# Kernel optimization log

Hardware: AMD Instinct MI355X
Metric: run time of the kernel (lower is better)

## Reference

```python
import jax, jax.numpy as jnp
import numpy as np

N_NODES = 100000
N_EDGES = 3200000
DROP_P = 0.5


def gcn_conv(x, W, b, src, dst, deg_inv_sqrt, n):
    # PyG GCNConv with self-loops already folded into (src, dst):
    # out[j] = sum_{(i->j)} dinv[i]*dinv[j] * (x W)[i] + b
    h = x @ W
    norm = deg_inv_sqrt[src] * deg_inv_sqrt[dst]          # [E+N]
    msg = h[src] * norm[:, None]                          # [E+N, d_out]
    out = jax.ops.segment_sum(msg, dst, num_segments=n)
    return out + b


def dropout(x, key, p=DROP_P):
    keep = jax.random.bernoulli(key, 1.0 - p, x.shape)
    return jnp.where(keep, x / (1.0 - p), 0.0)


def setup_inputs() -> dict:
    key = jax.random.key(0)
    ks = jax.random.split(key, 8)
    x = jax.random.normal(ks[0], (N_NODES, 64), dtype=jnp.float32)
    edge_index = jax.random.randint(ks[1], (2, N_EDGES), 0, N_NODES, dtype=jnp.int64)
    def glorot(k, fin, fout):
        lim = float(np.sqrt(6.0 / (fin + fout)))
        return jax.random.uniform(k, (fin, fout), jnp.float32, -lim, lim)
    return {
        "x": x,
        "edge_index": edge_index,
        "W1": glorot(ks[2], 64, 32), "b1": jnp.zeros((32,), jnp.float32),
        "W2": glorot(ks[3], 32, 64), "b2": jnp.zeros((64,), jnp.float32),
        "W3": glorot(ks[4], 64, 32), "b3": jnp.zeros((32,), jnp.float32),
    }


def reference(x, edge_index, W1, b1, W2, b2, W3, b3):
    n = x.shape[0]
    loops = jnp.arange(n, dtype=edge_index.dtype)
    src = jnp.concatenate([edge_index[0], loops])          # [E+N]
    dst = jnp.concatenate([edge_index[1], loops])
    deg = jax.ops.segment_sum(jnp.ones_like(dst, dtype=x.dtype), dst, num_segments=n)
    deg_inv_sqrt = jnp.where(deg > 0, jax.lax.rsqrt(deg), 0.0)

    dkey = jax.random.key(42)
    k1, k2 = jax.random.split(dkey)

    h = gcn_conv(x, W1, b1, src, dst, deg_inv_sqrt, n)
    h = jax.nn.celu(h)
    h = dropout(h, k1)
    h = gcn_conv(h, W2, b2, src, dst, deg_inv_sqrt, n)
    h = jax.nn.celu(h)
    h = dropout(h, k2)
    h = gcn_conv(h, W3, b3, src, dst, deg_inv_sqrt, n)
    return jax.nn.celu(h)
```

## Files before the change

kernel.cpp:

```cpp
#include <hip/hip_runtime.h>
#include <stdint.h>
#include <stddef.h>

typedef _Float16 half_t;
typedef _Float16 half4 __attribute__((ext_vector_type(4)));

__host__ __device__ __forceinline__ uint32_t rotl32(uint32_t v, uint32_t r) {
  return (v << r) | (v >> (32u - r));
}

__host__ __device__ __forceinline__ void tf2x32(uint32_t k0, uint32_t k1,
                                                uint32_t x0, uint32_t x1,
                                                uint32_t& o0, uint32_t& o1) {
  uint32_t ks2 = k0 ^ k1 ^ 0x1BD11BDAu;
  x0 += k0; x1 += k1;
  x0 += x1; x1 = rotl32(x1, 13); x1 ^= x0;
  x0 += x1; x1 = rotl32(x1, 15); x1 ^= x0;
  x0 += x1; x1 = rotl32(x1, 26); x1 ^= x0;
  x0 += x1; x1 = rotl32(x1, 6);  x1 ^= x0;
  x0 += k1; x1 += ks2 + 1u;
  x0 += x1; x1 = rotl32(x1, 17); x1 ^= x0;
  x0 += x1; x1 = rotl32(x1, 29); x1 ^= x0;
  x0 += x1; x1 = rotl32(x1, 16); x1 ^= x0;
  x0 += x1; x1 = rotl32(x1, 24); x1 ^= x0;
  x0 += ks2; x1 += k0 + 2u;
  x0 += x1; x1 = rotl32(x1, 13); x1 ^= x0;
  x0 += x1; x1 = rotl32(x1, 15); x1 ^= x0;
  x0 += x1; x1 = rotl32(x1, 26); x1 ^= x0;
  x0 += x1; x1 = rotl32(x1, 6);  x1 ^= x0;
  x0 += k0; x1 += k1 + 3u;
  x0 += x1; x1 = rotl32(x1, 17); x1 ^= x0;
  x0 += x1; x1 = rotl32(x1, 29); x1 ^= x0;
  x0 += x1; x1 = rotl32(x1, 16); x1 ^= x0;
  x0 += x1; x1 = rotl32(x1, 24); x1 ^= x0;
  x0 += k1; x1 += ks2 + 4u;
  x0 += x1; x1 = rotl32(x1, 13); x1 ^= x0;
  x0 += x1; x1 = rotl32(x1, 15); x1 ^= x0;
  x0 += x1; x1 = rotl32(x1, 26); x1 ^= x0;
  x0 += x1; x1 = rotl32(x1, 6);  x1 ^= x0;
  x0 += ks2; x1 += k0 + 5u;
  o0 = x0; o1 = x1;
}

__device__ __forceinline__ bool tf_keep(uint32_t k0, uint32_t k1, uint32_t idx) {
  uint32_t o0, o1;
  tf2x32(k0, k1, 0u, idx, o0, o1);
  return ((o0 ^ o1) >> 31) == 0u;
}

#define CHUNK 4096
#define STASH 5120

__global__ __launch_bounds__(1024) void zero1024(uint32_t* __restrict__ p) {
  p[threadIdx.x] = 0u;
}

__global__ __launch_bounds__(256) void k4_binhist(const int* __restrict__ src,
                                                  const int* __restrict__ dst,
                                                  uint32_t* __restrict__ tbl,
                                                  uint32_t* __restrict__ gbcnt,
                                                  uint32_t* __restrict__ staging,
                                                  int E, int NB) {
  __shared__ uint32_t lcur[1024];
  __shared__ uint32_t ls[256];
  __shared__ uint32_t stage[CHUNK];
  int tid = threadIdx.x;
  for (int i = tid; i < NB; i += 256) lcur[i] = 0u;
  __syncthreads();
  int base = blockIdx.x * CHUNK;
  int end = min(base + CHUNK, E);
  uint32_t dv[16], sv[16];
  int m = 0;
  for (int i = base + tid; i < end; i += 256) {
    dv[m] = (uint32_t)dst[i];
    sv[m] = (uint32_t)src[i];
    ++m;
  }
  for (int q = 0; q < m; ++q) atomicAdd(&lcur[dv[q] >> 7], 1u);
  __syncthreads();
  uint32_t carry = 0u;
  for (int seg = 0; seg < 1024; seg += 256) {
    int i = seg + tid;
    uint32_t v = (i < NB) ? lcur[i] : 0u;
    ls[tid] = v;
    __syncthreads();
    for (int off = 1; off < 256; off <<= 1) {
      uint32_t t = (tid >= off) ? ls[tid - off] : 0u;
      __syncthreads();
      if (tid >= off) ls[tid] += t;
      __syncthreads();
    }
    uint32_t excl = carry + ls[tid] - v;
    if (i < NB) {
      tbl[(size_t)blockIdx.x * NB + i] = (excl << 16) | v;
      if (v) atomicAdd(&gbcnt[i], v);
      lcur[i] = excl;
    }
    carry += ls[255];
    __syncthreads();
  }
  for (int q = 0; q < m; ++q) {
    uint32_t d = dv[q];
    uint32_t p = atomicAdd(&lcur[d >> 7], 1u);
    stage[p] = ((d & 127u) << 17) | sv[q];
  }
  __syncthreads();
  int cnt_total = end - base;
  uint32_t* outp = staging + (size_t)blockIdx.x * CHUNK;
  for (int i = tid; i < cnt_total; i += 256) outp[i] = stage[i];
}

__global__ __launch_bounds__(1024) void k3_bscan(const uint32_t* __restrict__ gbcnt,
                                                 uint32_t* __restrict__ bbase, int NB) {
  __shared__ uint32_t s[1024];
  int i = threadIdx.x;
  uint32_t v = (i < NB) ? gbcnt[i] : 0u;
  s[i] = v;
  __syncthreads();
  for (int off = 1; off < 1024; off <<= 1) {
    uint32_t t = (i >= off) ? s[i - off] : 0u;
    __syncthreads();
    if (i >= off) s[i] += t;
    __syncthreads();
  }
  if (i < NB) bbase[i] = s[i] - v;
}

__global__ __launch_bounds__(256) void k5_fin(
    const uint32_t* __restrict__ staging, const uint32_t* __restrict__ tbl,
    const uint32_t* __restrict__ bbase, uint32_t* __restrict__ rowp,
    float* __restrict__ dinv, uint32_t* __restrict__ esrc,
    int n, int E, int NBLK, int NB) {
  __shared__ uint32_t lpak[1024];
  __shared__ uint32_t P[1025];
  __shared__ uint32_t ls[256];
  __shared__ uint32_t stash[STASH];
  __shared__ uint32_t lc[128];
  __shared__ uint32_t sc[128];
  __shared__ uint32_t lcur[128];
  int tid = threadIdx.x;
  int b = blockIdx.x;
  if (tid < 128) lc[tid] = 0u;
  uint32_t carry = 0u;
  for (int seg = 0; seg < 1024; seg += 256) {
    int i = seg + tid;
    uint32_t packed = (i < NBLK) ? tbl[(size_t)i * NB + b] : 0u;
    lpak[i] = packed;
    uint32_t v = packed & 0xFFFFu;
    ls[tid] = v;
    __syncthreads();
    for (int off = 1; off < 256; off <<= 1) {
      uint32_t t = (tid >= off) ? ls[tid - off] : 0u;
      __syncthreads();
      if (tid >= off) ls[tid] += t;
      __syncthreads();
    }
    P[i] = carry + ls[tid] - v;
    carry += ls[255];
    __syncthreads();
  }
  if (tid == 0) P[NBLK] = carry;
  __syncthreads();
  uint32_t total = P[NBLK];
  for (int i = tid; i < NBLK; i += 256) {
    uint32_t packed = lpak[i];
    uint32_t cnt = packed & 0xFFFFu;
    uint32_t loff = packed >> 16;
    uint32_t p = P[i];
    const uint32_t* run = staging + (size_t)i * CHUNK + loff;
    for (uint32_t t2 = 0; t2 < cnt; ++t2) {
      uint32_t e = run[t2];
      uint32_t q = p + t2;
      if (q < STASH) stash[q] = e;
      atomicAdd(&lc[e >> 17], 1u);
    }
  }
  __syncthreads();
  uint32_t myc = (tid < 128) ? lc[tid] : 0u;
  if (tid < 128) sc[tid] = myc;
  __syncthreads();
  for (int off = 1; off < 128; off <<= 1) {
    uint32_t t = (tid < 128 && tid >= off) ? sc[tid - off] : 0u;
    __syncthreads();
    if (tid < 128 && tid >= off) sc[tid] += t;
    __syncthreads();
  }
  uint32_t s = bbase[b];
  if (tid < 128) {
    uint32_t gstart = s + sc[tid] - myc;
    int node = (b << 7) + tid;
    if (node < n) {
      rowp[node] = gstart;
      dinv[node] = 1.0f / sqrtf((float)(myc + 1u));
    }
    lcur[tid] = gstart;
  }
  if (b == 0 && tid == 0) rowp[n] = (uint32_t)E;
  __syncthreads();
  uint32_t lim = total < (uint32_t)STASH ? total : (uint32_t)STASH;
  for (uint32_t q = tid; q < lim; q += 256) {
    uint32_t e = stash[q];
    uint32_t pos = atomicAdd(&lcur[e >> 17], 1u);
    esrc[pos] = e & 0x1FFFFu;
  }
  if (total > (uint32_t)STASH) {
    for (int i = tid; i < NBLK; i += 256) {
      uint32_t packed = lpak[i];
      uint32_t cnt = packed & 0xFFFFu;
      uint32_t loff = packed >> 16;
      uint32_t p = P[i];
      const uint32_t* run = staging + (size_t)i * CHUNK + loff;
      for (uint32_t t2 = 0; t2 < cnt; ++t2) {
        uint32_t q = p + t2;
        if (q >= (uint32_t)STASH) {
          uint32_t e = run[t2];
          uint32_t pos = atomicAdd(&lcur[e >> 17], 1u);
          esrc[pos] = e & 0x1FFFFu;
        }
      }
    }
  }
}

__global__ __launch_bounds__(256) void gemm_n64_k32(
    const float* __restrict__ X, const float* __restrict__ W,
    const float* __restrict__ dinv, half_t* __restrict__ out16, int n) {
  __shared__ float Ws[64 * 32];
  __shared__ float Xs[32 * 68];
  int tid = threadIdx.x;
  {
    const float4* Wv = (const float4*)W;
    float4* Wsv = (float4*)Ws;
    Wsv[tid] = Wv[tid];
    Wsv[tid + 256] = Wv[tid + 256];
  }
  int row0 = blockIdx.x * 32;
  {
    const float4* Xv = (const float4*)(X + (size_t)row0 * 64);
    int lim = (n - row0) * 16;
    float4 z = make_float4(0.f, 0.f, 0.f, 0.f);
    int i0 = tid, i1 = tid + 256;
    float4 v0 = (i0 < lim) ? Xv[i0] : z;
    float4 v1 = (i1 < lim) ? Xv[i1] : z;
    *(float4*)(Xs + (i0 >> 4) * 68 + ((i0 & 15) << 2)) = v0;
    *(float4*)(Xs + (i1 >> 4) * 68 + ((i1 & 15) << 2)) = v1;
  }
  __syncthreads();
  int r = tid >> 3;
  int c4 = (tid & 7) << 2;
  int row = row0 + r;
  if (row >= n) return;
  float4 acc = make_float4(0.f, 0.f, 0.f, 0.f);
#pragma unroll
  for (int k = 0; k < 64; k += 4) {
    float4 xv = *(const float4*)(Xs + r * 68 + k);
    float4 w0 = *(const float4*)(Ws + (k + 0) * 32 + c4);
    float4 w1 = *(const float4*)(Ws + (k + 1) * 32 + c4);
    float4 w2 = *(const float4*)(Ws + (k + 2) * 32 + c4);
    float4 w3 = *(const float4*)(Ws + (k + 3) * 32 + c4);
    acc.x = fmaf(xv.x, w0.x, acc.x); acc.y = fmaf(xv.x, w0.y, acc.y);
    acc.z = fmaf(xv.x, w0.z, acc.z); acc.w = fmaf(xv.x, w0.w, acc.w);
    acc.x = fmaf(xv.y, w1.x, acc.x); acc.y = fmaf(xv.y, w1.y, acc.y);
    acc.z = fmaf(xv.y, w1.z, acc.z); acc.w = fmaf(xv.y, w1.w, acc.w);
    acc.x = fmaf(xv.z, w2.x, acc.x); acc.y = fmaf(xv.z, w2.y, acc.y);
    acc.z = fmaf(xv.z, w2.z, acc.z); acc.w = fmaf(xv.z, w2.w, acc.w);
    acc.x = fmaf(xv.w, w3.x, acc.x); acc.y = fmaf(xv.w, w3.y, acc.y);
    acc.z = fmaf(xv.w, w3.z, acc.z); acc.w = fmaf(xv.w, w3.w, acc.w);
  }
  float dj = dinv[row];
  half4 h;
  h.x = (half_t)(acc.x * dj); h.y = (half_t)(acc.y * dj);
  h.z = (half_t)(acc.z * dj); h.w = (half_t)(acc.w * dj);
  *(half4*)(out16 + (size_t)row * 32 + c4) = h;
}

__global__ __launch_bounds__(256) void gemm_k32_n64_act(
    const float* __restrict__ X, const float* __restrict__ W,
    const float* __restrict__ bias, float* __restrict__ out,
    uint32_t k0, uint32_t k1, int n) {
  __shared__ float Ws[32 * 64];
  __shared__ float Xs[16 * 36];
  int tid = threadIdx.x;
  {
    const float4* Wv = (const float4*)W;
    float4* Wsv = (float4*)Ws;
    Wsv[tid] = Wv[tid];
    Wsv[tid + 256] = Wv[tid + 256];
  }
  int row0 = blockIdx.x * 16;
  if (tid < 128) {
    const float4* Xv = (const float4*)(X + (size_t)row0 * 32);
    int lim = (n - row0) * 8;
    float4 z = make_float4(0.f, 0.f, 0.f, 0.f);
    float4 v = (tid < lim) ? Xv[tid] : z;
    *(float4*)(Xs + (tid >> 3) * 36 + ((tid & 7) << 2)) = v;
  }
  __syncthreads();
  int r = tid >> 4;
  int c4 = (tid & 15) << 2;
  int row = row0 + r;
  if (row >= n) return;
  float4 acc = make_float4(0.f, 0.f, 0.f, 0.f);
#pragma unroll
  for (int k = 0; k < 32; k += 4) {
    float4 xv = *(const float4*)(Xs + r * 36 + k);
    float4 w0 = *(const float4*)(Ws + (k + 0) * 64 + c4);
    float4 w1 = *(const float4*)(Ws + (k + 1) * 64 + c4);
    float4 w2 = *(const float4*)(Ws + (k + 2) * 64 + c4);
    float4 w3 = *(const float4*)(Ws + (k + 3) * 64 + c4);
    acc.x = fmaf(xv.x, w0.x, acc.x); acc.y = fmaf(xv.x, w0.y, acc.y);
    acc.z = fmaf(xv.x, w0.z, acc.z); acc.w = fmaf(xv.x, w0.w, acc.w);
    acc.x = fmaf(xv.y, w1.x, acc.x); acc.y = fmaf(xv.y, w1.y, acc.y);
    acc.z = fmaf(xv.y, w1.z, acc.z); acc.w = fmaf(xv.y, w1.w, acc.w);
    acc.x = fmaf(xv.z, w2.x, acc.x); acc.y = fmaf(xv.z, w2.y, acc.y);
    acc.z = fmaf(xv.z, w2.z, acc.z); acc.w = fmaf(xv.z, w2.w, acc.w);
    acc.x = fmaf(xv.w, w3.x, acc.x); acc.y = fmaf(xv.w, w3.y, acc.y);
    acc.z = fmaf(xv.w, w3.z, acc.z); acc.w = fmaf(xv.w, w3.w, acc.w);
  }
  float4 bv = *(const float4*)(bias + c4);
  float vv[4] = {acc.x + bv.x, acc.y + bv.y, acc.z + bv.z, acc.w + bv.w};
  uint32_t base = (uint32_t)row * 64u + (uint32_t)c4;
#pragma unroll
  for (int q = 0; q < 4; ++q) {
    float v = vv[q];
    v = v > 0.f ? v : expm1f(v);
    vv[q] = tf_keep(k0, k1, base + q) ? v * 2.f : 0.f;
  }
  *(float4*)(out + (size_t)row * 64 + c4) = make_float4(vv[0], vv[1], vv[2], vv[3]);
}

__global__ __launch_bounds__(256) void gather_fin(
    const half_t* __restrict__ hs, const uint32_t* __restrict__ rowp,
    const uint32_t* __restrict__ esrc, const float* __restrict__ dinv,
    const float* __restrict__ bias, float* __restrict__ outf,
    half_t* __restrict__ outh, int n, int mode, uint32_t k0, uint32_t k1) {
  int gt = blockIdx.x * 256 + threadIdx.x;
  int j = gt >> 5;
  if (j >= n) return;
  int l = threadIdx.x & 31;
  int eslot = l >> 3;
  int c4 = (l & 7) << 2;
  float4 acc = make_float4(0.f, 0.f, 0.f, 0.f);
  uint32_t e0 = rowp[j], e1 = rowp[j + 1];
  uint32_t deg = e1 - e0;
  uint32_t base = 0;
  for (; base + 32 <= deg; base += 32) {
    uint32_t idx = esrc[e0 + base + (uint32_t)l];
#pragma unroll
    for (int k = 0; k < 32; k += 4) {
      uint32_t s = (uint32_t)__shfl((int)idx, k + eslot, 32);
      const half4 v = *(const half4*)(hs + ((size_t)s << 5) + c4);
      acc.x += (float)v.x; acc.y += (float)v.y;
      acc.z += (float)v.z; acc.w += (float)v.w;
    }
  }
  if (base < deg) {
    uint32_t rem = deg - base;
    uint32_t li = (uint32_t)l < rem ? (uint32_t)l : rem - 1u;
    uint32_t idx = esrc[e0 + base + li];
    for (uint32_t k = 0; k < rem; k += 4) {
      uint32_t kk = k + (uint32_t)eslot;
      uint32_t ks = kk < rem ? kk : rem - 1u;
      uint32_t s = (uint32_t)__shfl((int)idx, (int)ks, 32);
      if (kk < rem) {
        const half4 v = *(const half4*)(hs + ((size_t)s << 5) + c4);
        acc.x += (float)v.x; acc.y += (float)v.y;
        acc.z += (float)v.z; acc.w += (float)v.w;
      }
    }
  }
  acc.x += __shfl_xor(acc.x, 8);  acc.y += __shfl_xor(acc.y, 8);
  acc.z += __shfl_xor(acc.z, 8);  acc.w += __shfl_xor(acc.w, 8);
  acc.x += __shfl_xor(acc.x, 16); acc.y += __shfl_xor(acc.y, 16);
  acc.z += __shfl_xor(acc.z, 16); acc.w += __shfl_xor(acc.w, 16);
  int srcLane = (threadIdx.x & 32) | (l >> 2);
  float va = __shfl(acc.x, srcLane);
  float vb = __shfl(acc.y, srcLane);
  float vc = __shfl(acc.z, srcLane);
  float vd = __shfl(acc.w, srcLane);
  float lo = (l & 1) ? vb : va;
  float hi = (l & 1) ? vd : vc;
  float sum = (l & 2) ? hi : lo;
  sum += (float)hs[gt];
  float dj = dinv[j];
  float v = dj * sum;
  if (mode == 1) {
    v += bias[l];
    v = v > 0.f ? v : expm1f(v);
    outf[gt] = v;
  } else if (mode == 3) {
    v += bias[l];
    v = v > 0.f ? v : expm1f(v);
    v = tf_keep(k0, k1, (uint32_t)gt) ? v * 2.f : 0.f;
    v *= dj;
    outh[gt] = (half_t)v;
  } else {
    outf[gt] = v;
  }
}

extern "C" void kernel_launch(void* const* d_in, const int* in_sizes, int n_in,
                              void* d_out, int out_size, void* d_ws, size_t ws_size,
                              hipStream_t stream) {
  const float* x  = (const float*)d_in[0];
  const int*   ei = (const int*)d_in[1];
  const float* W1 = (const float*)d_in[2];
  const float* b1 = (const float*)d_in[3];
  const float* W2 = (const float*)d_in[4];
  const float* b2 = (const float*)d_in[5];
  const float* W3 = (const float*)d_in[6];
  const float* b3 = (const float*)d_in[7];
  float* out = (float*)d_out;

  const int n = in_sizes[0] / 64;
  const int E = in_sizes[1] / 2;
  const int* src = ei;
  const int* dst = ei + E;

  char* ws = (char*)d_ws;
  size_t off = 0;
  auto alloc = [&](size_t bytes) {
    void* p = ws + off;
    off = (off + bytes + 255) & ~(size_t)255;
    return p;
  };
  float*    A32   = (float*)alloc((size_t)n * 32 * 4);
  float*    C     = (float*)alloc((size_t)n * 64 * 4);
  half_t*   A16   = (half_t*)alloc((size_t)n * 32 * 2);
  half_t*   B16   = (half_t*)alloc((size_t)n * 32 * 2);
  float*    dinv  = (float*)alloc((size_t)n * 4);
  uint32_t* rowp  = (uint32_t*)alloc((size_t)(n + 1) * 4);
  uint32_t* esrc  = (uint32_t*)alloc((size_t)E * 4);
  uint32_t* gbcnt = (uint32_t*)alloc(1024 * 4);
  uint32_t* bbase = (uint32_t*)alloc(1024 * 4);
  uint32_t* staging = (uint32_t*)C;
  uint32_t* tbl     = (uint32_t*)A32;
  (void)ws_size; (void)n_in; (void)out_size;

  uint32_t k1a, k1b, k2a, k2b;
  tf2x32(0u, 42u, 0u, 0u, k1a, k1b);
  tf2x32(0u, 42u, 0u, 1u, k2a, k2b);

  const int NB   = (n + 127) >> 7;
  const int NBLK = (E + CHUNK - 1) / CHUNK;
  const int nv   = n * 32;
  const int gV   = (nv + 255) / 256;
  const int gG1  = (n + 31) / 32;
  const int gG2  = (n + 15) / 16;
  dim3 blk(256);

  zero1024<<<1, dim3(1024), 0, stream>>>(gbcnt);
  k4_binhist<<<NBLK, blk, 0, stream>>>(src, dst, tbl, gbcnt, staging, E, NB);
  k3_bscan<<<1, dim3(1024), 0, stream>>>(gbcnt, bbase, NB);
  k5_fin<<<NB, blk, 0, stream>>>(staging, tbl, bbase, rowp, dinv, esrc, n, E, NBLK, NB);

  gemm_n64_k32<<<gG1, blk, 0, stream>>>(x, W1, dinv, A16, n);
  gather_fin<<<gV, blk, 0, stream>>>(A16, rowp, esrc, dinv, b1, nullptr, B16, n, 3, k1a, k1b);

  gather_fin<<<gV, blk, 0, stream>>>(B16, rowp, esrc, dinv, nullptr, A32, nullptr, n, 0, 0u, 0u);
  gemm_k32_n64_act<<<gG2, blk, 0, stream>>>(A32, W2, b2, C, k2a, k2b, n);

  gemm_n64_k32<<<gG1, blk, 0, stream>>>(C, W3, dinv, A16, n);
  gather_fin<<<gV, blk, 0, stream>>>(A16, rowp, esrc, dinv, b3, out, nullptr, n, 1, 0u, 0u);
}
```

Measured before the change: 347.9 us.

## Split half-precision node features into two 16-column slabs for gather locality

The fp16 feature buffers are stored as two column slabs of 16 halves per node instead of one 32-wide row. The gather kernel now assigns each block to one slab, with each destination row handled by 8 edge slots times 4 column chunks. Adjacent blocks are interleaved so that both column halves of the same destination range run close together. The goal is a smaller working set per pass, so random neighbour gathers hit cache better. In exchange, each destination's edge list is read twice, half the lanes go idle in the epilogue, and a wider shuffle reduction is needed.

```diff
diff --git a/kernel.cpp b/kernel.cpp
--- a/kernel.cpp
+++ b/kernel.cpp
@@ -271,7 +271,8 @@
   half4 h;
   h.x = (half_t)(acc.x * dj); h.y = (half_t)(acc.y * dj);
   h.z = (half_t)(acc.z * dj); h.w = (half_t)(acc.w * dj);
-  *(half4*)(out16 + (size_t)row * 32 + c4) = h;
+  size_t slab = (size_t)(c4 >> 4) * ((size_t)n * 16);
+  *(half4*)(out16 + slab + (size_t)row * 16 + (c4 & 15)) = h;
 }
 
 __global__ __launch_bounds__(256) void gemm_k32_n64_act(
@@ -334,12 +335,16 @@
     const uint32_t* __restrict__ esrc, const float* __restrict__ dinv,
     const float* __restrict__ bias, float* __restrict__ outf,
     half_t* __restrict__ outh, int n, int mode, uint32_t k0, uint32_t k1) {
-  int gt = blockIdx.x * 256 + threadIdx.x;
-  int j = gt >> 5;
+  uint32_t bid = blockIdx.x;
+  int cg = (int)((bid >> 2) & 1u);
+  int dstblk = (int)((bid >> 3) * 4u + (bid & 3u));
+  int tid = threadIdx.x;
+  int j = dstblk * 8 + (tid >> 5);
   if (j >= n) return;
-  int l = threadIdx.x & 31;
-  int eslot = l >> 3;
-  int c4 = (l & 7) << 2;
+  int l = tid & 31;
+  int eslot = l >> 2;
+  int chunk = l & 3;
+  const half_t* slab = hs + (size_t)cg * ((size_t)n * 16);
   float4 acc = make_float4(0.f, 0.f, 0.f, 0.f);
   uint32_t e0 = rowp[j], e1 = rowp[j + 1];
   uint32_t deg = e1 - e0;
@@ -347,9 +352,9 @@
   for (; base + 32 <= deg; base += 32) {
     uint32_t idx = esrc[e0 + base + (uint32_t)l];
 #pragma unroll
-    for (int k = 0; k < 32; k += 4) {
+    for (int k = 0; k < 32; k += 8) {
       uint32_t s = (uint32_t)__shfl((int)idx, k + eslot, 32);
-      const half4 v = *(const half4*)(hs + ((size_t)s << 5) + c4);
+      const half4 v = *(const half4*)(slab + (size_t)s * 16 + (chunk << 2));
       acc.x += (float)v.x; acc.y += (float)v.y;
       acc.z += (float)v.z; acc.w += (float)v.w;
     }
@@ -358,44 +363,47 @@
     uint32_t rem = deg - base;
     uint32_t li = (uint32_t)l < rem ? (uint32_t)l : rem - 1u;
     uint32_t idx = esrc[e0 + base + li];
-    for (uint32_t k = 0; k < rem; k += 4) {
+    for (uint32_t k = 0; k < rem; k += 8) {
       uint32_t kk = k + (uint32_t)eslot;
       uint32_t ks = kk < rem ? kk : rem - 1u;
       uint32_t s = (uint32_t)__shfl((int)idx, (int)ks, 32);
       if (kk < rem) {
-        const half4 v = *(const half4*)(hs + ((size_t)s << 5) + c4);
+        const half4 v = *(const half4*)(slab + (size_t)s * 16 + (chunk << 2));
         acc.x += (float)v.x; acc.y += (float)v.y;
         acc.z += (float)v.z; acc.w += (float)v.w;
       }
     }
   }
+  acc.x += __shfl_xor(acc.x, 4);  acc.y += __shfl_xor(acc.y, 4);
+  acc.z += __shfl_xor(acc.z, 4);  acc.w += __shfl_xor(acc.w, 4);
   acc.x += __shfl_xor(acc.x, 8);  acc.y += __shfl_xor(acc.y, 8);
   acc.z += __shfl_xor(acc.z, 8);  acc.w += __shfl_xor(acc.w, 8);
   acc.x += __shfl_xor(acc.x, 16); acc.y += __shfl_xor(acc.y, 16);
   acc.z += __shfl_xor(acc.z, 16); acc.w += __shfl_xor(acc.w, 16);
-  int srcLane = (threadIdx.x & 32) | (l >> 2);
-  float va = __shfl(acc.x, srcLane);
-  float vb = __shfl(acc.y, srcLane);
-  float vc = __shfl(acc.z, srcLane);
-  float vd = __shfl(acc.w, srcLane);
+  float va = __shfl(acc.x, l >> 2, 32);
+  float vb = __shfl(acc.y, l >> 2, 32);
+  float vc = __shfl(acc.z, l >> 2, 32);
+  float vd = __shfl(acc.w, l >> 2, 32);
+  if (l >= 16) return;
   float lo = (l & 1) ? vb : va;
   float hi = (l & 1) ? vd : vc;
   float sum = (l & 2) ? hi : lo;
-  sum += (float)hs[gt];
+  sum += (float)slab[(size_t)j * 16 + l];
+  int c = (cg << 4) | l;
   float dj = dinv[j];
   float v = dj * sum;
   if (mode == 1) {
-    v += bias[l];
+    v += bias[c];
     v = v > 0.f ? v : expm1f(v);
-    outf[gt] = v;
+    outf[(size_t)j * 32 + c] = v;
   } else if (mode == 3) {
-    v += bias[l];
+    v += bias[c];
     v = v > 0.f ? v : expm1f(v);
-    v = tf_keep(k0, k1, (uint32_t)gt) ? v * 2.f : 0.f;
+    v = tf_keep(k0, k1, (uint32_t)(j * 32 + c)) ? v * 2.f : 0.f;
     v *= dj;
-    outh[gt] = (half_t)v;
+    outh[(size_t)cg * ((size_t)n * 16) + (size_t)j * 16 + l] = (half_t)v;
   } else {
-    outf[gt] = v;
+    outf[(size_t)j * 32 + c] = v;
   }
 }
 
@@ -443,8 +451,8 @@
 
   const int NB   = (n + 127) >> 7;
   const int NBLK = (E + CHUNK - 1) / CHUNK;
-  const int nv   = n * 32;
-  const int gV   = (nv + 255) / 256;
+  const int NDB  = (n + 7) / 8;
+  const int gV2  = 8 * ((NDB + 3) / 4);
   const int gG1  = (n + 31) / 32;
   const int gG2  = (n + 15) / 16;
   dim3 blk(256);
@@ -455,11 +463,11 @@
   k5_fin<<<NB, blk, 0, stream>>>(staging, tbl, bbase, rowp, dinv, esrc, n, E, NBLK, NB);
 
   gemm_n64_k32<<<gG1, blk, 0, stream>>>(x, W1, dinv, A16, n);
-  gather_fin<<<gV, blk, 0, stream>>>(A16, rowp, esrc, dinv, b1, nullptr, B16, n, 3, k1a, k1b);
-
-  gather_fin<<<gV, blk, 0, stream>>>(B16, rowp, esrc, dinv, nullptr, A32, nullptr, n, 0, 0u, 0u);
+  gather_fin<<<gV2, blk, 0, stream>>>(A16, rowp, esrc, dinv, b1, nullptr, B16, n, 3, k1a, k1b);
+
+  gather_fin<<<gV2, blk, 0, stream>>>(B16, rowp, esrc, dinv, nullptr, A32, nullptr, n, 0, 0u, 0u);
   gemm_k32_n64_act<<<gG2, blk, 0, stream>>>(A32, W2, b2, C, k2a, k2b, n);
 
   gemm_n64_k32<<<gG1, blk, 0, stream>>>(C, W3, dinv, A16, n);
-  gather_fin<<<gV, blk, 0, stream>>>(A16, rowp, esrc, dinv, b3, out, nullptr, n, 1, 0u, 0u);
-}
+  gather_fin<<<gV2, blk, 0, stream>>>(A16, rowp, esrc, dinv, b3, out, nullptr, n, 1, 0u, 0u);
+}
```

Result: slower. 383.2 us (+10.2%).
